# Performance work log

Measured on AMD Instinct MI355X. Metric: run time of the kernel, lower is better.

Reference implementation:

```python
import jax, jax.numpy as jnp
import numpy as np

N = 50000
E = 800000
HEADS = 4
C = 64  # per-head channels
IN = 256
NEG_SLOPE = 0.2


def setup_inputs() -> dict:
    key = jax.random.key(0)
    k = jax.random.split(key, 6)
    x = jax.random.normal(k[0], (N, IN), dtype=jnp.float32)
    edge_index = jax.random.randint(k[1], (2, E), 0, N, dtype=jnp.int64)
    # Glorot-ish scale for weights
    W = jax.random.normal(k[2], (IN, HEADS * C), dtype=jnp.float32) * (1.0 / np.sqrt(IN))
    att_src = jax.random.normal(k[3], (HEADS, C), dtype=jnp.float32) * (1.0 / np.sqrt(C))
    att_dst = jax.random.normal(k[4], (HEADS, C), dtype=jnp.float32) * (1.0 / np.sqrt(C))
    bias = jax.random.normal(k[5], (HEADS * C,), dtype=jnp.float32) * 0.02
    return {"x": x, "edge_index": edge_index, "W": W, "att_src": att_src,
            "att_dst": att_dst, "bias": bias}


def _gat_forward(x, edge_index, W, att_src, att_dst, bias):
    n = x.shape[0]
    h = (x @ W).reshape(n, HEADS, C)  # [N, H, C]

    # add self loops (PyG default add_self_loops=True)
    loop = jnp.arange(n, dtype=edge_index.dtype)
    src = jnp.concatenate([edge_index[0], loop])  # [E+N]
    dst = jnp.concatenate([edge_index[1], loop])

    # per-node attention contributions  [N, H]
    a_src = jnp.einsum('nhc,hc->nh', h, att_src)
    a_dst = jnp.einsum('nhc,hc->nh', h, att_dst)

    # edge logits with leaky relu  [E+N, H]
    logits = a_src[src] + a_dst[dst]
    logits = jnp.where(logits >= 0, logits, NEG_SLOPE * logits)

    # segment softmax over destination neighborhoods
    seg_max = jax.ops.segment_max(logits, dst, num_segments=n)  # [N, H]
    seg_max = jnp.where(jnp.isfinite(seg_max), seg_max, 0.0)
    ex = jnp.exp(logits - seg_max[dst])
    denom = jax.ops.segment_sum(ex, dst, num_segments=n)  # [N, H]
    alpha = ex / (denom[dst] + 1e-16)  # [E+N, H]

    # weighted scatter-add of source messages
    msgs = alpha[:, :, None] * h[src]  # [E+N, H, C]
    out = jax.ops.segment_sum(msgs, dst, num_segments=n)  # [N, H, C]
    out = out.reshape(n, HEADS * C) + bias
    return jax.nn.relu(out)


def reference(x, edge_index, W, att_src, att_dst, bias):
    return _gat_forward(x, edge_index, W, att_src, att_dst, bias)
```

## Files before the change

kernel.cpp:

```cpp
#include <hip/hip_runtime.h>
#include <hip/hip_bf16.h>
#include <math.h>

#define NEG 0.2f
#define BSH 6
#define EPB 2048

typedef __attribute__((ext_vector_type(4))) float f4;
typedef __attribute__((ext_vector_type(8))) short s8;

__device__ __forceinline__ short f2bf(float f) {
    unsigned u = __float_as_uint(f);
    u += 0x7fff + ((u >> 16) & 1);
    return (short)(u >> 16);
}
__device__ __forceinline__ unsigned pk2(float a, float b) {
    union { __hip_bfloat162 h; unsigned u; } c;
    c.h = __float22bfloat162_rn(make_float2(a, b));
    return c.u;
}
__device__ __forceinline__ float bf2f(unsigned short s) {
    return __uint_as_float(((unsigned)s) << 16);
}

__global__ __launch_bounds__(256) void prep_count(
    const float* __restrict__ W, short* __restrict__ Wt, int* __restrict__ off,
    const int* __restrict__ ei, int* __restrict__ hist2d,
    int E, int N, int NBUCK, int NB, int Etot)
{
    const int blk = blockIdx.x, t = threadIdx.x;
    if (blk < 256) {
        int id = blk * 256 + t;
        int n = id >> 8, k = id & 255;
        Wt[id] = f2bf(W[k * 256 + n]);
        if (id == 0) off[N] = Etot;
        return;
    }
    extern __shared__ int lh[];
    const int cblk = blk - 256;
    for (int b = t; b < NBUCK; b += 256) lh[b] = 0;
    __syncthreads();
    const int e0 = cblk * EPB;
    if (e0 + EPB <= E) {
#pragma unroll
        for (int i = 0; i < EPB / 1024; ++i) {
            int e = e0 + i * 1024 + t * 4;
            int4 d = *(const int4*)(ei + E + e);
            atomicAdd(&lh[d.x >> BSH], 1);
            atomicAdd(&lh[d.y >> BSH], 1);
            atomicAdd(&lh[d.z >> BSH], 1);
            atomicAdd(&lh[d.w >> BSH], 1);
        }
    } else {
        for (int i = 0; i < EPB / 256; ++i) {
            int e = e0 + i * 256 + t;
            if (e < Etot) {
                int dte = (e < E) ? ei[E + e] : (e - E);
                atomicAdd(&lh[dte >> BSH], 1);
            }
        }
    }
    __syncthreads();
    for (int b = t; b < NBUCK; b += 256) hist2d[b * NB + cblk] = lh[b];
}

__global__ __launch_bounds__(512) void gemm_attn(
    const float* __restrict__ x, const short* __restrict__ Wt,
    const float* __restrict__ att_src, const float* __restrict__ att_dst,
    short* __restrict__ hb, float* __restrict__ a_src_n,
    float* __restrict__ a_dst_n, int M)
{
    __shared__ __align__(16) short xs[2][128][32];
    const int t = threadIdx.x;
    const int lane = t & 63, wv = t >> 6;
    const int wr = wv >> 2;
    const int hd = wv & 3;
    const int quad = lane >> 4, l15 = lane & 15;
    const int n0 = blockIdx.x * 128;

    const int row = t >> 2, kq = t & 3;
    const bool okr = (n0 + row) < M;
    const float* xp = x + (size_t)(n0 + row) * 256 + kq * 8;

    const short* wbase = Wt + (size_t)(hd * 64 + l15) * 256 + quad * 8;

    f4 acc[4][4];
#pragma unroll
    for (int i = 0; i < 4; ++i)
#pragma unroll
        for (int j = 0; j < 4; ++j) acc[i][j] = (f4)(0.f);

    float4 v0 = {}, v1 = {};
    if (okr) { const float4* p = (const float4*)xp; v0 = p[0]; v1 = p[1]; }

    s8 af[4];
#pragma unroll
    for (int i = 0; i < 4; ++i)
        af[i] = *(const s8*)(wbase + (size_t)(i * 16) * 256);

    int buf = 0;
#pragma unroll
    for (int ks = 0; ks < 8; ++ks) {
        uint4 u = { pk2(v0.x, v0.y), pk2(v0.z, v0.w), pk2(v1.x, v1.y), pk2(v1.z, v1.w) };
        *(uint4*)&xs[buf][row][kq * 8] = u;
        __syncthreads();

        if (ks < 7 && okr) {
            const float4* p = (const float4*)(xp + (ks + 1) * 32);
            v0 = p[0]; v1 = p[1];
        }

        s8 afn[4];
        if (ks < 7) {
#pragma unroll
            for (int i = 0; i < 4; ++i)
                afn[i] = *(const s8*)(wbase + (size_t)(i * 16) * 256 + (ks + 1) * 32);
        }

        s8 bf[4];
#pragma unroll
        for (int j = 0; j < 4; ++j)
            bf[j] = *(const s8*)&xs[buf][wr * 64 + j * 16 + l15][quad * 8];
#pragma unroll
        for (int i = 0; i < 4; ++i)
#pragma unroll
            for (int j = 0; j < 4; ++j)
                acc[i][j] = __builtin_amdgcn_mfma_f32_16x16x32_bf16(af[i], bf[j], acc[i][j], 0, 0, 0);

        if (ks < 7) {
#pragma unroll
            for (int i = 0; i < 4; ++i) af[i] = afn[i];
        }
        buf ^= 1;
    }

    float asv[4][4], adv[4][4];
#pragma unroll
    for (int i = 0; i < 4; ++i)
#pragma unroll
        for (int rr = 0; rr < 4; ++rr) {
            asv[i][rr] = att_src[hd * 64 + i * 16 + quad * 4 + rr];
            adv[i][rr] = att_dst[hd * 64 + i * 16 + quad * 4 + rr];
        }

#pragma unroll
    for (int j = 0; j < 4; ++j) {
        const int node = n0 + wr * 64 + j * 16 + l15;
        const bool ok = node < M;
        float ps = 0.f, pd = 0.f;
#pragma unroll
        for (int i = 0; i < 4; ++i)
#pragma unroll
            for (int rr = 0; rr < 4; ++rr) {
                float v = acc[i][j][rr];
                ps = fmaf(v, asv[i][rr], ps);
                pd = fmaf(v, adv[i][rr], pd);
            }
        ps += __shfl_xor(ps, 16); ps += __shfl_xor(ps, 32);
        pd += __shfl_xor(pd, 16); pd += __shfl_xor(pd, 32);
        if (ok && quad == 0) {
            a_src_n[node * 4 + hd] = ps;
            a_dst_n[node * 4 + hd] = pd;
        }
        if (ok) {
#pragma unroll
            for (int i = 0; i < 4; ++i) {
                uint2 pk = make_uint2(pk2(acc[i][j][0], acc[i][j][1]),
                                      pk2(acc[i][j][2], acc[i][j][3]));
                *(uint2*)&hb[(size_t)node * 256 + hd * 64 + i * 16 + quad * 4] = pk;
            }
        }
    }
}

__global__ __launch_bounds__(1024) void scan1(const int* __restrict__ src,
                                              int* __restrict__ dst,
                                              int* __restrict__ bsum, int Ntot)
{
    __shared__ int wsum[16], wexc[16];
    const int t = threadIdx.x, lane = t & 63, w = t >> 6;
    const int idx = blockIdx.x * 1024 + t;
    int v = (idx < Ntot) ? src[idx] : 0;
    int val = v;
#pragma unroll
    for (int o = 1; o < 64; o <<= 1) {
        int u = __shfl_up(val, o);
        if (lane >= o) val += u;
    }
    if (lane == 63) wsum[w] = val;
    __syncthreads();
    if (t < 16) {
        int s = wsum[t];
#pragma unroll
        for (int o = 1; o < 16; o <<= 1) {
            int u = __shfl_up(s, o, 16);
            if (t >= o) s += u;
        }
        wexc[t] = s - wsum[t];
        if (t == 15) bsum[blockIdx.x] = s;
    }
    __syncthreads();
    if (idx < Ntot) dst[idx] = wexc[w] + val - v;
}

__global__ __launch_bounds__(1024) void scan2v(const int* __restrict__ bsum,
                                               int* __restrict__ bexc, int nb)
{
    __shared__ int wsum[16], wexc[16];
    const int t = threadIdx.x, lane = t & 63, w = t >> 6;
    int v = (t < nb) ? bsum[t] : 0;
    int val = v;
#pragma unroll
    for (int o = 1; o < 64; o <<= 1) {
        int u = __shfl_up(val, o);
        if (lane >= o) val += u;
    }
    if (lane == 63) wsum[w] = val;
    __syncthreads();
    if (t < 16) {
        int s = wsum[t];
#pragma unroll
        for (int o = 1; o < 16; o <<= 1) {
            int u = __shfl_up(s, o, 16);
            if (t >= o) s += u;
        }
        wexc[t] = s - wsum[t];
    }
    __syncthreads();
    if (t < nb) bexc[t] = wexc[w] + val - v;
}

__global__ __launch_bounds__(256) void scatter2(const int* __restrict__ ei,
                                                const int* __restrict__ scanned,
                                                const int* __restrict__ bexc,
                                                unsigned* __restrict__ bucketed,
                                                int E, int N, int NBUCK, int NB)
{
    extern __shared__ int lcur[];
    const int t = threadIdx.x, blk = blockIdx.x;
    for (int b = t; b < NBUCK; b += 256) {
        int idx = b * NB + blk;
        lcur[b] = scanned[idx] + bexc[idx >> 10];
    }
    __syncthreads();
    const int e0 = blk * EPB, Etot = E + N;
    if (e0 + EPB <= E) {
#pragma unroll
        for (int i = 0; i < EPB / 1024; ++i) {
            int e = e0 + i * 1024 + t * 4;
            int4 s4 = *(const int4*)(ei + e);
            int4 d4 = *(const int4*)(ei + E + e);
            int p0 = atomicAdd(&lcur[d4.x >> BSH], 1);
            bucketed[p0] = (unsigned)s4.x | ((unsigned)(d4.x & 63) << 20);
            int p1 = atomicAdd(&lcur[d4.y >> BSH], 1);
            bucketed[p1] = (unsigned)s4.y | ((unsigned)(d4.y & 63) << 20);
            int p2 = atomicAdd(&lcur[d4.z >> BSH], 1);
            bucketed[p2] = (unsigned)s4.z | ((unsigned)(d4.z & 63) << 20);
            int p3 = atomicAdd(&lcur[d4.w >> BSH], 1);
            bucketed[p3] = (unsigned)s4.w | ((unsigned)(d4.w & 63) << 20);
        }
    } else {
        for (int i = 0; i < EPB / 256; ++i) {
            int e = e0 + i * 256 + t;
            if (e < Etot) {
                int src, dte;
                if (e < E) { src = ei[e]; dte = ei[E + e]; }
                else       { src = e - E; dte = src; }
                int pos = atomicAdd(&lcur[dte >> BSH], 1);
                bucketed[pos] = (unsigned)src | ((unsigned)(dte & 63) << 20);
            }
        }
    }
}

__global__ __launch_bounds__(256) void csr_build(
    const unsigned* __restrict__ bucketed, const int* __restrict__ scanned,
    const int* __restrict__ bexc, int* __restrict__ off, int* __restrict__ csr,
    int N, int NB, int NBUCK, int Etot)
{
    __shared__ unsigned est[2048];
    __shared__ int ldeg4[4][64], lcur4[4][64], loff[64];
    const int t = threadIdx.x, wv = t >> 6, b = blockIdx.x;

    const int i0 = b * NB;
    const int gbase = scanned[i0] + bexc[i0 >> 10];
    int gend;
    if (b + 1 == NBUCK) gend = Etot;
    else { int i1 = (b + 1) * NB; gend = scanned[i1] + bexc[i1 >> 10]; }
    int cnt = gend - gbase;
    if (cnt > 2048) cnt = 2048;

    ldeg4[t >> 6][t & 63] = 0;
    __syncthreads();
    for (int i = t; i < cnt; i += 256) {
        unsigned en = bucketed[gbase + i];
        est[i] = en;
        atomicAdd(&ldeg4[wv][en >> 20], 1);
    }
    __syncthreads();
    if (t < 64) {
        int d0 = ldeg4[0][t], d1 = ldeg4[1][t], d2 = ldeg4[2][t], d3 = ldeg4[3][t];
        int tot = d0 + d1 + d2 + d3;
        int val = tot;
#pragma unroll
        for (int o = 1; o < 64; o <<= 1) {
            int u = __shfl_up(val, o);
            if (t >= o) val += u;
        }
        int excl = val - tot;
        loff[t] = excl;
        lcur4[0][t] = excl;
        lcur4[1][t] = excl + d0;
        lcur4[2][t] = excl + d0 + d1;
        lcur4[3][t] = excl + d0 + d1 + d2;
    }
    __syncthreads();
    for (int i = t; i < cnt; i += 256) {
        unsigned en = est[i];
        int pos = atomicAdd(&lcur4[wv][en >> 20], 1);
        csr[gbase + pos] = (int)(en & 0xFFFFF);
    }
    if (t < 64) {
        int n = (b << BSH) + t;
        if (n < N) off[n] = gbase + loff[t];
    }
}

__global__ __launch_bounds__(256) void aggregate(const short* __restrict__ hb,
                                                 const float* __restrict__ a_src_n,
                                                 const float* __restrict__ a_dst_n,
                                                 const int* __restrict__ off,
                                                 const int* __restrict__ csr,
                                                 const float* __restrict__ bias,
                                                 float* __restrict__ out, int N)
{
    __shared__ float lds_w[4][64][4];
    __shared__ int   lds_s[4][64];
    const int wv = threadIdx.x >> 6;
    const int lane = threadIdx.x & 63;
    const int half = lane >> 5, l31 = lane & 31;
    const int hl = l31 >> 3;
    const uint4* hp = (const uint4*)hb;
    const int nstep = gridDim.x << 2;

    for (int n = blockIdx.x * 4 + wv; n < N; n += nstep) {
        const int base = off[n];
        const int d = off[n + 1] - base;
        const float4 ad = *(const float4*)(a_dst_n + 4 * n);

        float acc[8] = {0.f, 0.f, 0.f, 0.f, 0.f, 0.f, 0.f, 0.f};
        float4 sum = make_float4(0.f, 0.f, 0.f, 0.f);

        for (int c0 = 0; c0 < d; c0 += 64) {
            int j = c0 + lane;
            int s = 0;
            float4 w4 = make_float4(0.f, 0.f, 0.f, 0.f);
            if (j < d) {
                s = csr[base + j];
                float4 as = *(const float4*)(a_src_n + 4 * s);
                float lx = as.x + ad.x; lx = lx >= 0.f ? lx : NEG * lx;
                float ly = as.y + ad.y; ly = ly >= 0.f ? ly : NEG * ly;
                float lz = as.z + ad.z; lz = lz >= 0.f ? lz : NEG * lz;
                float lw = as.w + ad.w; lw = lw >= 0.f ? lw : NEG * lw;
                w4 = make_float4(__expf(lx), __expf(ly), __expf(lz), __expf(lw));
            }
            sum.x += w4.x; sum.y += w4.y; sum.z += w4.z; sum.w += w4.w;
            *(float4*)&lds_w[wv][lane][0] = w4;
            lds_s[wv][lane] = s;
            __builtin_amdgcn_wave_barrier();

            const int cl = (d - c0) < 64 ? (d - c0) : 64;
            int jj = 0;
            for (; jj + 4 <= cl; jj += 4) {
                int   s0 = lds_s[wv][jj + half];
                int   s1 = lds_s[wv][jj + 2 + half];
                float w0 = lds_w[wv][jj + half][hl];
                float w1 = lds_w[wv][jj + 2 + half][hl];
                uint4 v0 = hp[(size_t)s0 * 32 + l31];
                uint4 v1 = hp[(size_t)s1 * 32 + l31];
                acc[0] = fmaf(w0, bf2f((unsigned short)(v0.x & 0xffff)), acc[0]);
                acc[1] = fmaf(w0, bf2f((unsigned short)(v0.x >> 16)),    acc[1]);
                acc[2] = fmaf(w0, bf2f((unsigned short)(v0.y & 0xffff)), acc[2]);
                acc[3] = fmaf(w0, bf2f((unsigned short)(v0.y >> 16)),    acc[3]);
                acc[4] = fmaf(w0, bf2f((unsigned short)(v0.z & 0xffff)), acc[4]);
                acc[5] = fmaf(w0, bf2f((unsigned short)(v0.z >> 16)),    acc[5]);
                acc[6] = fmaf(w0, bf2f((unsigned short)(v0.w & 0xffff)), acc[6]);
                acc[7] = fmaf(w0, bf2f((unsigned short)(v0.w >> 16)),    acc[7]);
                acc[0] = fmaf(w1, bf2f((unsigned short)(v1.x & 0xffff)), acc[0]);
                acc[1] = fmaf(w1, bf2f((unsigned short)(v1.x >> 16)),    acc[1]);
                acc[2] = fmaf(w1, bf2f((unsigned short)(v1.y & 0xffff)), acc[2]);
                acc[3] = fmaf(w1, bf2f((unsigned short)(v1.y >> 16)),    acc[3]);
                acc[4] = fmaf(w1, bf2f((unsigned short)(v1.z & 0xffff)), acc[4]);
                acc[5] = fmaf(w1, bf2f((unsigned short)(v1.z >> 16)),    acc[5]);
                acc[6] = fmaf(w1, bf2f((unsigned short)(v1.w & 0xffff)), acc[6]);
                acc[7] = fmaf(w1, bf2f((unsigned short)(v1.w >> 16)),    acc[7]);
            }
            for (; jj < cl; jj += 2) {
                int   s0 = lds_s[wv][jj + half];
                float w0 = lds_w[wv][jj + half][hl];
                uint4 v0 = hp[(size_t)s0 * 32 + l31];
                acc[0] = fmaf(w0, bf2f((unsigned short)(v0.x & 0xffff)), acc[0]);
                acc[1] = fmaf(w0, bf2f((unsigned short)(v0.x >> 16)),    acc[1]);
                acc[2] = fmaf(w0, bf2f((unsigned short)(v0.y & 0xffff)), acc[2]);
                acc[3] = fmaf(w0, bf2f((unsigned short)(v0.y >> 16)),    acc[3]);
                acc[4] = fmaf(w0, bf2f((unsigned short)(v0.z & 0xffff)), acc[4]);
                acc[5] = fmaf(w0, bf2f((unsigned short)(v0.z >> 16)),    acc[5]);
                acc[6] = fmaf(w0, bf2f((unsigned short)(v0.w & 0xffff)), acc[6]);
                acc[7] = fmaf(w0, bf2f((unsigned short)(v0.w >> 16)),    acc[7]);
            }
            __builtin_amdgcn_wave_barrier();
        }

#pragma unroll
        for (int k = 0; k < 8; ++k) acc[k] += __shfl_xor(acc[k], 32);

#pragma unroll
        for (int o = 32; o > 0; o >>= 1) {
            sum.x += __shfl_xor(sum.x, o);
            sum.y += __shfl_xor(sum.y, o);
            sum.z += __shfl_xor(sum.z, o);
            sum.w += __shfl_xor(sum.w, o);
        }
        float sh = (hl & 2) ? ((hl & 1) ? sum.w : sum.z) : ((hl & 1) ? sum.y : sum.x);
        float ih = 1.f / (sh + 1e-16f);

        if (half == 0) {
            const float4* bp = (const float4*)bias + l31 * 2;
            float4 b0 = bp[0], b1 = bp[1];
            float4 o0, o1;
            o0.x = fmaxf(fmaf(acc[0], ih, b0.x), 0.f);
            o0.y = fmaxf(fmaf(acc[1], ih, b0.y), 0.f);
            o0.z = fmaxf(fmaf(acc[2], ih, b0.z), 0.f);
            o0.w = fmaxf(fmaf(acc[3], ih, b0.w), 0.f);
            o1.x = fmaxf(fmaf(acc[4], ih, b1.x), 0.f);
            o1.y = fmaxf(fmaf(acc[5], ih, b1.y), 0.f);
            o1.z = fmaxf(fmaf(acc[6], ih, b1.z), 0.f);
            o1.w = fmaxf(fmaf(acc[7], ih, b1.w), 0.f);
            float4* op = (float4*)(out + (size_t)n * 256) + l31 * 2;
            op[0] = o0;
            op[1] = o1;
        }
    }
}

extern "C" void kernel_launch(void* const* d_in, const int* in_sizes, int n_in,
                              void* d_out, int out_size, void* d_ws, size_t ws_size,
                              hipStream_t stream)
{
    const float* x       = (const float*)d_in[0];
    const int*   ei      = (const int*)d_in[1];
    const float* W       = (const float*)d_in[2];
    const float* att_src = (const float*)d_in[3];
    const float* att_dst = (const float*)d_in[4];
    const float* bias    = (const float*)d_in[5];
    float* out = (float*)d_out;

    const int N = in_sizes[0] / 256;
    const int E = in_sizes[1] / 2;
    const int Etot = E + N;
    const int NBUCK = (N + 63) >> BSH;
    const int NB = (Etot + EPB - 1) / EPB;
    const int Ntot = NBUCK * NB;
    const int nb1 = (Ntot + 1023) / 1024;

    char* p = (char*)d_ws;
    short*    hb      = (short*)p;    p += (size_t)N * 256 * sizeof(short);
    short*    Wt      = (short*)p;    p += 256 * 256 * sizeof(short);
    float*    a_src_n = (float*)p;    p += (size_t)N * 4 * sizeof(float);
    float*    a_dst_n = (float*)p;    p += (size_t)N * 4 * sizeof(float);
    int*      hist2d  = (int*)p;      p += (size_t)Ntot * sizeof(int);
    int*      scanned = (int*)p;      p += (size_t)Ntot * sizeof(int);
    int*      bsum    = (int*)p;      p += 1024 * sizeof(int);
    int*      bexc    = (int*)p;      p += 1024 * sizeof(int);
    int*      off     = (int*)p;      p += (size_t)(N + 1) * sizeof(int);
    unsigned* bucketed= (unsigned*)p; p += (size_t)Etot * sizeof(unsigned);
    int*      csr     = (int*)p;      p += (size_t)Etot * sizeof(int);

    prep_count<<<256 + NB, 256, NBUCK * sizeof(int), stream>>>(
        W, Wt, off, ei, hist2d, E, N, NBUCK, NB, Etot);
    gemm_attn<<<(N + 127) / 128, 512, 0, stream>>>(
        x, Wt, att_src, att_dst, hb, a_src_n, a_dst_n, N);
    scan1<<<nb1, 1024, 0, stream>>>(hist2d, scanned, bsum, Ntot);
    scan2v<<<1, 1024, 0, stream>>>(bsum, bexc, nb1);
    scatter2<<<NB, 256, NBUCK * sizeof(int), stream>>>(ei, scanned, bexc, bucketed,
                                                       E, N, NBUCK, NB);
    csr_build<<<NBUCK, 256, 0, stream>>>(bucketed, scanned, bexc, off, csr,
                                         N, NB, NBUCK, Etot);
    aggregate<<<2048, 256, 0, stream>>>(hb, a_src_n, a_dst_n, off, csr,
                                        bias, out, N);
}
```

Baseline: 239.6 us.

## Fuse GEMM with edge scatter in one launch and use one-node-per-wave aggregate grid

Merges the feature-transform GEMM kernel and the bucket scatter kernel into a single launch. Extra blocks beyond the GEMM grid do the scatter work, so the two independent stages can overlap on the GPU and one launch is dropped. The scans are moved ahead of the fused kernel. The aggregate kernel switches from a grid-stride loop over 2048 blocks to one wave per node with a full-size grid. The fused kernel uses a uniform 16KB dynamic shared allocation, which must hold both the GEMM tile and the NBUCK bucket counters (782 ints for N=50000). This could limit occupancy for the scatter blocks.

After: 215.1 us. 10.2% less time.

```diff
diff --git a/kernel.cpp b/kernel.cpp
--- a/kernel.cpp
+++ b/kernel.cpp
@@ -64,14 +64,112 @@
     for (int b = t; b < NBUCK; b += 256) hist2d[b * NB + cblk] = lh[b];
 }
 
-__global__ __launch_bounds__(512) void gemm_attn(
+__global__ __launch_bounds__(1024) void scan1(const int* __restrict__ src,
+                                              int* __restrict__ dst,
+                                              int* __restrict__ bsum, int Ntot)
+{
+    __shared__ int wsum[16], wexc[16];
+    const int t = threadIdx.x, lane = t & 63, w = t >> 6;
+    const int idx = blockIdx.x * 1024 + t;
+    int v = (idx < Ntot) ? src[idx] : 0;
+    int val = v;
+#pragma unroll
+    for (int o = 1; o < 64; o <<= 1) {
+        int u = __shfl_up(val, o);
+        if (lane >= o) val += u;
+    }
+    if (lane == 63) wsum[w] = val;
+    __syncthreads();
+    if (t < 16) {
+        int s = wsum[t];
+#pragma unroll
+        for (int o = 1; o < 16; o <<= 1) {
+            int u = __shfl_up(s, o, 16);
+            if (t >= o) s += u;
+        }
+        wexc[t] = s - wsum[t];
+        if (t == 15) bsum[blockIdx.x] = s;
+    }
+    __syncthreads();
+    if (idx < Ntot) dst[idx] = wexc[w] + val - v;
+}
+
+__global__ __launch_bounds__(1024) void scan2v(const int* __restrict__ bsum,
+                                               int* __restrict__ bexc, int nb)
+{
+    __shared__ int wsum[16], wexc[16];
+    const int t = threadIdx.x, lane = t & 63, w = t >> 6;
+    int v = (t < nb) ? bsum[t] : 0;
+    int val = v;
+#pragma unroll
+    for (int o = 1; o < 64; o <<= 1) {
+        int u = __shfl_up(val, o);
+        if (lane >= o) val += u;
+    }
+    if (lane == 63) wsum[w] = val;
+    __syncthreads();
+    if (t < 16) {
+        int s = wsum[t];
+#pragma unroll
+        for (int o = 1; o < 16; o <<= 1) {
+            int u = __shfl_up(s, o, 16);
+            if (t >= o) s += u;
+        }
+        wexc[t] = s - wsum[t];
+    }
+    __syncthreads();
+    if (t < nb) bexc[t] = wexc[w] + val - v;
+}
+
+__global__ __launch_bounds__(512) void gemm_scatter(
     const float* __restrict__ x, const short* __restrict__ Wt,
     const float* __restrict__ att_src, const float* __restrict__ att_dst,
     short* __restrict__ hb, float* __restrict__ a_src_n,
-    float* __restrict__ a_dst_n, int M)
-{
-    __shared__ __align__(16) short xs[2][128][32];
+    float* __restrict__ a_dst_n, int M, int GB,
+    const int* __restrict__ ei, const int* __restrict__ scanned,
+    const int* __restrict__ bexc, unsigned* __restrict__ bucketed,
+    int E, int N, int NBUCK, int NB)
+{
+    extern __shared__ __align__(16) char smem[];
     const int t = threadIdx.x;
+
+    if (blockIdx.x >= GB) {
+        int* lcur = (int*)smem;
+        const int cblk = blockIdx.x - GB;
+        for (int b = t; b < NBUCK; b += 512) {
+            int idx = b * NB + cblk;
+            lcur[b] = scanned[idx] + bexc[idx >> 10];
+        }
+        __syncthreads();
+        const int e0 = cblk * EPB, Etot = E + N;
+        if (e0 + EPB <= E) {
+            int e = e0 + t * 4;
+            int4 s4 = *(const int4*)(ei + e);
+            int4 d4 = *(const int4*)(ei + E + e);
+            int p0 = atomicAdd(&lcur[d4.x >> BSH], 1);
+            bucketed[p0] = (unsigned)s4.x | ((unsigned)(d4.x & 63) << 20);
+            int p1 = atomicAdd(&lcur[d4.y >> BSH], 1);
+            bucketed[p1] = (unsigned)s4.y | ((unsigned)(d4.y & 63) << 20);
+            int p2 = atomicAdd(&lcur[d4.z >> BSH], 1);
+            bucketed[p2] = (unsigned)s4.z | ((unsigned)(d4.z & 63) << 20);
+            int p3 = atomicAdd(&lcur[d4.w >> BSH], 1);
+            bucketed[p3] = (unsigned)s4.w | ((unsigned)(d4.w & 63) << 20);
+        } else {
+            for (int i = 0; i < EPB / 512; ++i) {
+                int e = e0 + i * 512 + t;
+                if (e < Etot) {
+                    int src, dte;
+                    if (e < E) { src = ei[e]; dte = ei[E + e]; }
+                    else       { src = e - E; dte = src; }
+                    int pos = atomicAdd(&lcur[dte >> BSH], 1);
+                    bucketed[pos] = (unsigned)src | ((unsigned)(dte & 63) << 20);
+                }
+            }
+        }
+        return;
+    }
+
+    short (*xs)[128][32] = (short (*)[128][32])smem;
     const int lane = t & 63, wv = t >> 6;
     const int wr = wv >> 2;
     const int hd = wv & 3;
@@ -173,106 +271,6 @@
     }
 }
 
-__global__ __launch_bounds__(1024) void scan1(const int* __restrict__ src,
-                                              int* __restrict__ dst,
-                                              int* __restrict__ bsum, int Ntot)
-{
-    __shared__ int wsum[16], wexc[16];
-    const int t = threadIdx.x, lane = t & 63, w = t >> 6;
-    const int idx = blockIdx.x * 1024 + t;
-    int v = (idx < Ntot) ? src[idx] : 0;
-    int val = v;
-#pragma unroll
-    for (int o = 1; o < 64; o <<= 1) {
-        int u = __shfl_up(val, o);
-        if (lane >= o) val += u;
-    }
-    if (lane == 63) wsum[w] = val;
-    __syncthreads();
-    if (t < 16) {
-        int s = wsum[t];
-#pragma unroll
-        for (int o = 1; o < 16; o <<= 1) {
-            int u = __shfl_up(s, o, 16);
-            if (t >= o) s += u;
-        }
-        wexc[t] = s - wsum[t];
-        if (t == 15) bsum[blockIdx.x] = s;
-    }
-    __syncthreads();
-    if (idx < Ntot) dst[idx] = wexc[w] + val - v;
-}
-
-__global__ __launch_bounds__(1024) void scan2v(const int* __restrict__ bsum,
-                                               int* __restrict__ bexc, int nb)
-{
-    __shared__ int wsum[16], wexc[16];
-    const int t = threadIdx.x, lane = t & 63, w = t >> 6;
-    int v = (t < nb) ? bsum[t] : 0;
-    int val = v;
-#pragma unroll
-    for (int o = 1; o < 64; o <<= 1) {
-        int u = __shfl_up(val, o);
-        if (lane >= o) val += u;
-    }
-    if (lane == 63) wsum[w] = val;
-    __syncthreads();
-    if (t < 16) {
-        int s = wsum[t];
-#pragma unroll
-        for (int o = 1; o < 16; o <<= 1) {
-            int u = __shfl_up(s, o, 16);
-            if (t >= o) s += u;
-        }
-        wexc[t] = s - wsum[t];
-    }
-    __syncthreads();
-    if (t < nb) bexc[t] = wexc[w] + val - v;
-}
-
-__global__ __launch_bounds__(256) void scatter2(const int* __restrict__ ei,
-                                                const int* __restrict__ scanned,
-                                                const int* __restrict__ bexc,
-                                                unsigned* __restrict__ bucketed,
-                                                int E, int N, int NBUCK, int NB)
-{
-    extern __shared__ int lcur[];
-    const int t = threadIdx.x, blk = blockIdx.x;
-    for (int b = t; b < NBUCK; b += 256) {
-        int idx = b * NB + blk;
-        lcur[b] = scanned[idx] + bexc[idx >> 10];
-    }
-    __syncthreads();
-    const int e0 = blk * EPB, Etot = E + N;
-    if (e0 + EPB <= E) {
-#pragma unroll
-        for (int i = 0; i < EPB / 1024; ++i) {
-            int e = e0 + i * 1024 + t * 4;
-            int4 s4 = *(const int4*)(ei + e);
-            int4 d4 = *(const int4*)(ei + E + e);
-            int p0 = atomicAdd(&lcur[d4.x >> BSH], 1);
-            bucketed[p0] = (unsigned)s4.x | ((unsigned)(d4.x & 63) << 20);
-            int p1 = atomicAdd(&lcur[d4.y >> BSH], 1);
-            bucketed[p1] = (unsigned)s4.y | ((unsigned)(d4.y & 63) << 20);
-            int p2 = atomicAdd(&lcur[d4.z >> BSH], 1);
-            bucketed[p2] = (unsigned)s4.z | ((unsigned)(d4.z & 63) << 20);
-            int p3 = atomicAdd(&lcur[d4.w >> BSH], 1);
-            bucketed[p3] = (unsigned)s4.w | ((unsigned)(d4.w & 63) << 20);
-        }
-    } else {
-        for (int i = 0; i < EPB / 256; ++i) {
-            int e = e0 + i * 256 + t;
-            if (e < Etot) {
-                int src, dte;
-                if (e < E) { src = ei[e]; dte = ei[E + e]; }
-                else       { src = e - E; dte = src; }
-                int pos = atomicAdd(&lcur[dte >> BSH], 1);
-                bucketed[pos] = (unsigned)src | ((unsigned)(dte & 63) << 20);
-            }
-        }
-    }
-}
-
 __global__ __launch_bounds__(256) void csr_build(
     const unsigned* __restrict__ bucketed, const int* __restrict__ scanned,
     const int* __restrict__ bexc, int* __restrict__ off, int* __restrict__ csr,
@@ -339,107 +337,106 @@
     const int wv = threadIdx.x >> 6;
     const int lane = threadIdx.x & 63;
     const int half = lane >> 5, l31 = lane & 31;
+    const int n = blockIdx.x * 4 + wv;
+    if (n >= N) return;
+
+    const int base = off[n];
+    const int d = off[n + 1] - base;
+    const float4 ad = *(const float4*)(a_dst_n + 4 * n);
     const int hl = l31 >> 3;
+
+    float acc[8] = {0.f, 0.f, 0.f, 0.f, 0.f, 0.f, 0.f, 0.f};
+    float4 sum = make_float4(0.f, 0.f, 0.f, 0.f);
     const uint4* hp = (const uint4*)hb;
-    const int nstep = gridDim.x << 2;
-
-    for (int n = blockIdx.x * 4 + wv; n < N; n += nstep) {
-        const int base = off[n];
-        const int d = off[n + 1] - base;
-        const float4 ad = *(const float4*)(a_dst_n + 4 * n);
-
-        float acc[8] = {0.f, 0.f, 0.f, 0.f, 0.f, 0.f, 0.f, 0.f};
-        float4 sum = make_float4(0.f, 0.f, 0.f, 0.f);
-
-        for (int c0 = 0; c0 < d; c0 += 64) {
-            int j = c0 + lane;
-            int s = 0;
-            float4 w4 = make_float4(0.f, 0.f, 0.f, 0.f);
-            if (j < d) {
-                s = csr[base + j];
-                float4 as = *(const float4*)(a_src_n + 4 * s);
-                float lx = as.x + ad.x; lx = lx >= 0.f ? lx : NEG * lx;
-                float ly = as.y + ad.y; ly = ly >= 0.f ? ly : NEG * ly;
-                float lz = as.z + ad.z; lz = lz >= 0.f ? lz : NEG * lz;
-                float lw = as.w + ad.w; lw = lw >= 0.f ? lw : NEG * lw;
-                w4 = make_float4(__expf(lx), __expf(ly), __expf(lz), __expf(lw));
-            }
-            sum.x += w4.x; sum.y += w4.y; sum.z += w4.z; sum.w += w4.w;
-            *(float4*)&lds_w[wv][lane][0] = w4;
-            lds_s[wv][lane] = s;
-            __builtin_amdgcn_wave_barrier();
-
-            const int cl = (d - c0) < 64 ? (d - c0) : 64;
-            int jj = 0;
-            for (; jj + 4 <= cl; jj += 4) {
-                int   s0 = lds_s[wv][jj + half];
-                int   s1 = lds_s[wv][jj + 2 + half];
-                float w0 = lds_w[wv][jj + half][hl];
-                float w1 = lds_w[wv][jj + 2 + half][hl];
-                uint4 v0 = hp[(size_t)s0 * 32 + l31];
-                uint4 v1 = hp[(size_t)s1 * 32 + l31];
-                acc[0] = fmaf(w0, bf2f((unsigned short)(v0.x & 0xffff)), acc[0]);
-                acc[1] = fmaf(w0, bf2f((unsigned short)(v0.x >> 16)),    acc[1]);
-                acc[2] = fmaf(w0, bf2f((unsigned short)(v0.y & 0xffff)), acc[2]);
-                acc[3] = fmaf(w0, bf2f((unsigned short)(v0.y >> 16)),    acc[3]);
-                acc[4] = fmaf(w0, bf2f((unsigned short)(v0.z & 0xffff)), acc[4]);
-                acc[5] = fmaf(w0, bf2f((unsigned short)(v0.z >> 16)),    acc[5]);
-                acc[6] = fmaf(w0, bf2f((unsigned short)(v0.w & 0xffff)), acc[6]);
-                acc[7] = fmaf(w0, bf2f((unsigned short)(v0.w >> 16)),    acc[7]);
-                acc[0] = fmaf(w1, bf2f((unsigned short)(v1.x & 0xffff)), acc[0]);
-                acc[1] = fmaf(w1, bf2f((unsigned short)(v1.x >> 16)),    acc[1]);
-                acc[2] = fmaf(w1, bf2f((unsigned short)(v1.y & 0xffff)), acc[2]);
-                acc[3] = fmaf(w1, bf2f((unsigned short)(v1.y >> 16)),    acc[3]);
-                acc[4] = fmaf(w1, bf2f((unsigned short)(v1.z & 0xffff)), acc[4]);
-                acc[5] = fmaf(w1, bf2f((unsigned short)(v1.z >> 16)),    acc[5]);
-                acc[6] = fmaf(w1, bf2f((unsigned short)(v1.w & 0xffff)), acc[6]);
-                acc[7] = fmaf(w1, bf2f((unsigned short)(v1.w >> 16)),    acc[7]);
-            }
-            for (; jj < cl; jj += 2) {
-                int   s0 = lds_s[wv][jj + half];
-                float w0 = lds_w[wv][jj + half][hl];
-                uint4 v0 = hp[(size_t)s0 * 32 + l31];
-                acc[0] = fmaf(w0, bf2f((unsigned short)(v0.x & 0xffff)), acc[0]);
-                acc[1] = fmaf(w0, bf2f((unsigned short)(v0.x >> 16)),    acc[1]);
-                acc[2] = fmaf(w0, bf2f((unsigned short)(v0.y & 0xffff)), acc[2]);
-                acc[3] = fmaf(w0, bf2f((unsigned short)(v0.y >> 16)),    acc[3]);
-                acc[4] = fmaf(w0, bf2f((unsigned short)(v0.z & 0xffff)), acc[4]);
-                acc[5] = fmaf(w0, bf2f((unsigned short)(v0.z >> 16)),    acc[5]);
-                acc[6] = fmaf(w0, bf2f((unsigned short)(v0.w & 0xffff)), acc[6]);
-                acc[7] = fmaf(w0, bf2f((unsigned short)(v0.w >> 16)),    acc[7]);
-            }
-            __builtin_amdgcn_wave_barrier();
-        }
-
-#pragma unroll
-        for (int k = 0; k < 8; ++k) acc[k] += __shfl_xor(acc[k], 32);
-
-#pragma unroll
-        for (int o = 32; o > 0; o >>= 1) {
-            sum.x += __shfl_xor(sum.x, o);
-            sum.y += __shfl_xor(sum.y, o);
-            sum.z += __shfl_xor(sum.z, o);
-            sum.w += __shfl_xor(sum.w, o);
-        }
-        float sh = (hl & 2) ? ((hl & 1) ? sum.w : sum.z) : ((hl & 1) ? sum.y : sum.x);
-        float ih = 1.f / (sh + 1e-16f);
-
-        if (half == 0) {
-            const float4* bp = (const float4*)bias + l31 * 2;
-            float4 b0 = bp[0], b1 = bp[1];
-            float4 o0, o1;
-            o0.x = fmaxf(fmaf(acc[0], ih, b0.x), 0.f);
-            o0.y = fmaxf(fmaf(acc[1], ih, b0.y), 0.f);
-            o0.z = fmaxf(fmaf(acc[2], ih, b0.z), 0.f);
-            o0.w = fmaxf(fmaf(acc[3], ih, b0.w), 0.f);
-            o1.x = fmaxf(fmaf(acc[4], ih, b1.x), 0.f);
-            o1.y = fmaxf(fmaf(acc[5], ih, b1.y), 0.f);
-            o1.z = fmaxf(fmaf(acc[6], ih, b1.z), 0.f);
-            o1.w = fmaxf(fmaf(acc[7], ih, b1.w), 0.f);
-            float4* op = (float4*)(out + (size_t)n * 256) + l31 * 2;
-            op[0] = o0;
-            op[1] = o1;
-        }
+
+    for (int c0 = 0; c0 < d; c0 += 64) {
+        int j = c0 + lane;
+        int s = 0;
+        float4 w4 = make_float4(0.f, 0.f, 0.f, 0.f);
+        if (j < d) {
+            s = csr[base + j];
+            float4 as = *(const float4*)(a_src_n + 4 * s);
+            float lx = as.x + ad.x; lx = lx >= 0.f ? lx : NEG * lx;
+            float ly = as.y + ad.y; ly = ly >= 0.f ? ly : NEG * ly;
+            float lz = as.z + ad.z; lz = lz >= 0.f ? lz : NEG * lz;
+            float lw = as.w + ad.w; lw = lw >= 0.f ? lw : NEG * lw;
+            w4 = make_float4(__expf(lx), __expf(ly), __expf(lz), __expf(lw));
+        }
+        sum.x += w4.x; sum.y += w4.y; sum.z += w4.z; sum.w += w4.w;
+        *(float4*)&lds_w[wv][lane][0] = w4;
+        lds_s[wv][lane] = s;
+        __builtin_amdgcn_wave_barrier();
+
+        const int cl = (d - c0) < 64 ? (d - c0) : 64;
+        int jj = 0;
+        for (; jj + 4 <= cl; jj += 4) {
+            int   s0 = lds_s[wv][jj + half];
+            int   s1 = lds_s[wv][jj + 2 + half];
+            float w0 = lds_w[wv][jj + half][hl];
+            float w1 = lds_w[wv][jj + 2 + half][hl];
+            uint4 v0 = hp[(size_t)s0 * 32 + l31];
+            uint4 v1 = hp[(size_t)s1 * 32 + l31];
+            acc[0] = fmaf(w0, bf2f((unsigned short)(v0.x & 0xffff)), acc[0]);
+            acc[1] = fmaf(w0, bf2f((unsigned short)(v0.x >> 16)),    acc[1]);
+            acc[2] = fmaf(w0, bf2f((unsigned short)(v0.y & 0xffff)), acc[2]);
+            acc[3] = fmaf(w0, bf2f((unsigned short)(v0.y >> 16)),    acc[3]);
+            acc[4] = fmaf(w0, bf2f((unsigned short)(v0.z & 0xffff)), acc[4]);
+            acc[5] = fmaf(w0, bf2f((unsigned short)(v0.z >> 16)),    acc[5]);
+            acc[6] = fmaf(w0, bf2f((unsigned short)(v0.w & 0xffff)), acc[6]);
+            acc[7] = fmaf(w0, bf2f((unsigned short)(v0.w >> 16)),    acc[7]);
+            acc[0] = fmaf(w1, bf2f((unsigned short)(v1.x & 0xffff)), acc[0]);
+            acc[1] = fmaf(w1, bf2f((unsigned short)(v1.x >> 16)),    acc[1]);
+            acc[2] = fmaf(w1, bf2f((unsigned short)(v1.y & 0xffff)), acc[2]);
+            acc[3] = fmaf(w1, bf2f((unsigned short)(v1.y >> 16)),    acc[3]);
+            acc[4] = fmaf(w1, bf2f((unsigned short)(v1.z & 0xffff)), acc[4]);
+            acc[5] = fmaf(w1, bf2f((unsigned short)(v1.z >> 16)),    acc[5]);
+            acc[6] = fmaf(w1, bf2f((unsigned short)(v1.w & 0xffff)), acc[6]);
+            acc[7] = fmaf(w1, bf2f((unsigned short)(v1.w >> 16)),    acc[7]);
+        }
+        for (; jj < cl; jj += 2) {
+            int   s0 = lds_s[wv][jj + half];
+            float w0 = lds_w[wv][jj + half][hl];
+            uint4 v0 = hp[(size_t)s0 * 32 + l31];
+            acc[0] = fmaf(w0, bf2f((unsigned short)(v0.x & 0xffff)), acc[0]);
+            acc[1] = fmaf(w0, bf2f((unsigned short)(v0.x >> 16)),    acc[1]);
+            acc[2] = fmaf(w0, bf2f((unsigned short)(v0.y & 0xffff)), acc[2]);
+            acc[3] = fmaf(w0, bf2f((unsigned short)(v0.y >> 16)),    acc[3]);
+            acc[4] = fmaf(w0, bf2f((unsigned short)(v0.z & 0xffff)), acc[4]);
+            acc[5] = fmaf(w0, bf2f((unsigned short)(v0.z >> 16)),    acc[5]);
+            acc[6] = fmaf(w0, bf2f((unsigned short)(v0.w & 0xffff)), acc[6]);
+            acc[7] = fmaf(w0, bf2f((unsigned short)(v0.w >> 16)),    acc[7]);
+        }
+        __builtin_amdgcn_wave_barrier();
+    }
+
+#pragma unroll
+    for (int k = 0; k < 8; ++k) acc[k] += __shfl_xor(acc[k], 32);
+
+#pragma unroll
+    for (int o = 32; o > 0; o >>= 1) {
+        sum.x += __shfl_xor(sum.x, o);
+        sum.y += __shfl_xor(sum.y, o);
+        sum.z += __shfl_xor(sum.z, o);
+        sum.w += __shfl_xor(sum.w, o);
+    }
+    float sh = (hl & 2) ? ((hl & 1) ? sum.w : sum.z) : ((hl & 1) ? sum.y : sum.x);
+    float ih = 1.f / (sh + 1e-16f);
+
+    if (half == 0) {
+        const float4* bp = (const float4*)bias + l31 * 2;
+        float4 b0 = bp[0], b1 = bp[1];
+        float4 o0, o1;
+        o0.x = fmaxf(fmaf(acc[0], ih, b0.x), 0.f);
+        o0.y = fmaxf(fmaf(acc[1], ih, b0.y), 0.f);
+        o0.z = fmaxf(fmaf(acc[2], ih, b0.z), 0.f);
+        o0.w = fmaxf(fmaf(acc[3], ih, b0.w), 0.f);
+        o1.x = fmaxf(fmaf(acc[4], ih, b1.x), 0.f);
+        o1.y = fmaxf(fmaf(acc[5], ih, b1.y), 0.f);
+        o1.z = fmaxf(fmaf(acc[6], ih, b1.z), 0.f);
+        o1.w = fmaxf(fmaf(acc[7], ih, b1.w), 0.f);
+        float4* op = (float4*)(out + (size_t)n * 256) + l31 * 2;
+        op[0] = o0;
+        op[1] = o1;
     }
 }
 
@@ -462,6 +459,7 @@
     const int NB = (Etot + EPB - 1) / EPB;
     const int Ntot = NBUCK * NB;
     const int nb1 = (Ntot + 1023) / 1024;
+    const int GB = (N + 127) / 128;
 
     char* p = (char*)d_ws;
     short*    hb      = (short*)p;    p += (size_t)N * 256 * sizeof(short);
@@ -478,14 +476,13 @@
 
     prep_count<<<256 + NB, 256, NBUCK * sizeof(int), stream>>>(
         W, Wt, off, ei, hist2d, E, N, NBUCK, NB, Etot);
-    gemm_attn<<<(N + 127) / 128, 512, 0, stream>>>(
-        x, Wt, att_src, att_dst, hb, a_src_n, a_dst_n, N);
     scan1<<<nb1, 1024, 0, stream>>>(hist2d, scanned, bsum, Ntot);
     scan2v<<<1, 1024, 0, stream>>>(bsum, bexc, nb1);
-    scatter2<<<NB, 256, NBUCK * sizeof(int), stream>>>(ei, scanned, bexc, bucketed,
-                                                       E, N, NBUCK, NB);
+    gemm_scatter<<<GB + NB, 512, 16384, stream>>>(
+        x, Wt, att_src, att_dst, hb, a_src_n, a_dst_n, N, GB,
+        ei, scanned, bexc, bucketed, E, N, NBUCK, NB);
     csr_build<<<NBUCK, 256, 0, stream>>>(bucketed, scanned, bexc, off, csr,
                                          N, NB, NBUCK, Etot);
-    aggregate<<<2048, 256, 0, stream>>>(hb, a_src_n, a_dst_n, off, csr,
-                                        bias, out, N);
-}
+    aggregate<<<(N + 3) / 4, 256, 0, stream>>>(hb, a_src_n, a_dst_n, off, csr,
+                                               bias, out, N);
+}
```
